# Optimization experiments

Hardware: AMD Instinct MI355X
Metric: run time of the kernel (lower is better)

Reference implementation:

```python
import jax, jax.numpy as jnp
import numpy as np

# --- config mirroring Prediction(__init__) ---
NUM_CLS = 3        # heatmap channels; total C = NUM_CLS + 2 (offset) + 2 (wh)
TOPK = 100         # peaks kept per stack output
SCALE = 4.0        # scale_factor: feature-map stride
CONF_TH = 0.1      # conf_th (also soft-NMS keep thresh, as in forward())
SIGMA = 0.5        # soft-NMS gaussian sigma (default in soft_nms_pytorch)


def setup_inputs() -> dict:
    key = jax.random.key(0)
    # network is identity => x is the raw head output (B, S, C, H, W)
    x = jax.random.normal(key, (32, 2, NUM_CLS + 4, 256, 256), dtype=jnp.float32)
    return {"x": x}


def _decode(hm, off, wh):
    """CenterNet-style hm2box: hm (C,H,W) post-sigmoid, off/wh (2,H,W)."""
    C, H, W = hm.shape
    scores, idx = jax.lax.top_k(hm.reshape(-1), TOPK)      # over C*H*W
    cls = idx // (H * W)
    rem = idx % (H * W)                                    # spatial flat index
    ys = (rem // W).astype(jnp.float32)
    xs = (rem % W).astype(jnp.float32)
    offx = off[0].reshape(-1)[rem]
    offy = off[1].reshape(-1)[rem]
    bw = wh[0].reshape(-1)[rem] * SCALE
    bh = wh[1].reshape(-1)[rem] * SCALE
    cx = (xs + offx) * SCALE
    cy = (ys + offy) * SCALE
    boxes = jnp.stack([cx - bw / 2, cy - bh / 2, cx + bw / 2, cy + bh / 2], axis=-1)
    # conf_th filter: zero-out low scores (fixed shape stand-in for boolean select)
    scores = jnp.where(scores > CONF_TH, scores, 0.0)
    return boxes, cls, scores


def _soft_nms(boxes, scores):
    """Faithful port of soft_nms_pytorch: sequential max-swap + gaussian decay."""
    N = boxes.shape[0]
    pos = jnp.arange(N)

    def step(carry, i):
        bxs, scs, idxs = carry
        # argmax over scores[i:] (includes i; strict '<' in original == first-max here)
        m = jnp.argmax(jnp.where(pos >= i, scs, -jnp.inf))

        def swap(a):
            ai, am = a[i], a[m]
            return a.at[i].set(am).at[m].set(ai)

        bxs, scs, idxs = swap(bxs), swap(scs), swap(idxs)
        bi = bxs[i]
        x1, y1, x2, y2 = bxs[:, 0], bxs[:, 1], bxs[:, 2], bxs[:, 3]
        areas = (x2 - x1 + 1.0) * (y2 - y1 + 1.0)
        area_i = (bi[2] - bi[0] + 1.0) * (bi[3] - bi[1] + 1.0)
        xx1 = jnp.maximum(bi[0], x1)
        yy1 = jnp.maximum(bi[1], y1)
        xx2 = jnp.minimum(bi[2], x2)
        yy2 = jnp.minimum(bi[3], y2)
        inter = jnp.maximum(0.0, xx2 - xx1 + 1.0) * jnp.maximum(0.0, yy2 - yy1 + 1.0)
        iou = inter / (area_i + areas - inter)
        w = jnp.exp(-(iou * iou) / SIGMA)
        scs = jnp.where(pos > i, w * scs, scs)   # decay only positions after i
        return (bxs, scs, idxs), None

    (bxs, scs, idxs), _ = jax.lax.scan(step, (boxes, scores, jnp.arange(N)), jnp.arange(N))
    keep = scs > CONF_TH
    return bxs, scs, idxs, keep


def reference(x):
    b, s, c, H, W = x.shape
    hm = jax.nn.sigmoid(x[:, :, :NUM_CLS])
    off = x[:, :, NUM_CLS:NUM_CLS + 2]
    wh = x[:, :, NUM_CLS + 2:]
    boxes, clss, scores = jax.vmap(jax.vmap(_decode))(hm, off, wh)
    boxes = boxes.reshape(b, s * TOPK, 4)
    clss = clss.reshape(b, s * TOPK)
    scores = scores.reshape(b, s * TOPK)
    nboxes, nscores, idxs, keep = jax.vmap(_soft_nms)(boxes, scores)
    nclss = jnp.take_along_axis(clss, idxs, axis=1)
    # fixed-shape outputs; `keep` marks the boxes the original would return
    return nboxes, nclss, nscores, keep
```

## Files before the change

kernel.cpp:

```cpp
#include <hip/hip_runtime.h>
#include <math.h>

#define TOPK 100
#define HW 65536
#define SLICE_STRIDE (7*HW)
#define NBATCH 32
#define NBOX 200
#define HM (3*HW)
#define CAP 4096
#define NPART 8
#define PPART 64
#define KEYS_BASE 256
#define WS_NEED ((size_t)(2048 + 64 * NPART * PPART * 8))
#define TKEYS 0xC0400000u

__device__ __forceinline__ unsigned fkey(float f) {
    unsigned u = __float_as_uint(f);
    return (u & 0x80000000u) ? ~u : (u | 0x80000000u);
}

__device__ __forceinline__ float sel4(const float a[4], int s) {
    float r = a[0];
    r = (s == 1) ? a[1] : r;
    r = (s == 2) ? a[2] : r;
    r = (s == 3) ? a[3] : r;
    return r;
}

#if defined(__has_builtin) && __has_builtin(__builtin_amdgcn_update_dpp)
#define DPP64_STEP(ctrl)                                                        \
    {                                                                           \
        unsigned lo = (unsigned)x, hi = (unsigned)(x >> 32);                    \
        unsigned olo = (unsigned)__builtin_amdgcn_update_dpp((int)lo, (int)lo,  \
                                                             (ctrl), 0xF, 0xF, false); \
        unsigned ohi = (unsigned)__builtin_amdgcn_update_dpp((int)hi, (int)hi,  \
                                                             (ctrl), 0xF, 0xF, false); \
        unsigned long long o = ((unsigned long long)ohi << 32) | olo;           \
        x = (o > x) ? o : x;                                                    \
    }
__device__ __forceinline__ unsigned long long wave_umax64(unsigned long long x) {
    DPP64_STEP(0x111) DPP64_STEP(0x112) DPP64_STEP(0x114)
    DPP64_STEP(0x118) DPP64_STEP(0x142) DPP64_STEP(0x143)
    unsigned rlo = (unsigned)__builtin_amdgcn_readlane((int)(unsigned)x, 63);
    unsigned rhi = (unsigned)__builtin_amdgcn_readlane((int)(unsigned)(x >> 32), 63);
    return ((unsigned long long)rhi << 32) | rlo;
}
__device__ __forceinline__ float lane_getf(const float a[4], int slot, int lane) {
    return __uint_as_float((unsigned)__builtin_amdgcn_readlane(
        (int)__float_as_uint(sel4(a, slot)), lane));
}
#else
__device__ __forceinline__ unsigned long long wave_umax64(unsigned long long x) {
    #pragma unroll
    for (int off = 32; off > 0; off >>= 1) {
        unsigned long long o = __shfl_xor(x, off);
        if (o > x) x = o;
    }
    return x;
}
__device__ __forceinline__ float lane_getf(const float a[4], int slot, int lane) {
    return __shfl(sel4(a, slot), lane);
}
#endif

typedef __attribute__((ext_vector_type(4))) float f4v;
#if defined(__has_builtin) && __has_builtin(__builtin_nontemporal_load)
#define NT_LOAD(p) __builtin_nontemporal_load(p)
#else
#define NT_LOAD(p) (*(p))
#endif

__global__ __launch_bounds__(1024) void kcollect(const float* __restrict__ x,
                                                 unsigned long long* __restrict__ ws) {
    __shared__ unsigned shCnt;
    const int bid = blockIdx.x;
    const int slice = bid >> 3, part = bid & 7;
    const int t = threadIdx.x;
    const float* xb = x + (size_t)slice * SLICE_STRIDE;
    const f4v* xb4 = (const f4v*)xb;
    unsigned* cnt = (unsigned*)ws;
    unsigned long long* keys = ws + KEYS_BASE;

    if (t == 0) shCnt = 0u;
    __syncthreads();

    const int i0 = part * (HM / 4 / NPART);
    const int i1 = i0 + (HM / 4 / NPART);
    for (int i = i0 + t; i < i1; i += 1024) {
        f4v v = NT_LOAD(&xb4[i]);
        float a[4] = {v.x, v.y, v.z, v.w};
        #pragma unroll
        for (int q = 0; q < 4; ++q) {
            unsigned vk = fkey(a[q]);
            if (vk >= TKEYS) {
                unsigned pos = atomicAdd(&shCnt, 1u);
                if (pos < PPART)
                    keys[(size_t)slice * (NPART * PPART) + part * PPART + pos] =
                        ((unsigned long long)vk << 32) |
                        (unsigned)~(unsigned)(i * 4 + q);
            }
        }
    }
    __syncthreads();
    if (t == 0) cnt[slice * NPART + part] = shCnt;
}

__device__ void fb_select(const float* xb, unsigned long long* fkrow,
                          unsigned* selmask, float* rv, int* ri, int t) {
    for (int i = t; i < HM / 32; i += 1024) selmask[i] = 0u;
    __syncthreads();
    for (int r = 0; r < TOPK; ++r) {
        float bv = -INFINITY; int bi = 0x7FFFFFFF;
        for (int i = t; i < HM; i += 1024) {
            if (!((selmask[i >> 5] >> (i & 31)) & 1u)) {
                float v = xb[i];
                if (v > bv || (v == bv && i < bi)) { bv = v; bi = i; }
            }
        }
        rv[t] = bv; ri[t] = bi;
        __syncthreads();
        for (int off = 512; off > 0; off >>= 1) {
            if (t < off) {
                float ov = rv[t + off]; int oi = ri[t + off];
                if (ov > rv[t] || (ov == rv[t] && oi < ri[t])) { rv[t] = ov; ri[t] = oi; }
            }
            __syncthreads();
        }
        if (t == 0) {
            int w = ri[0];
            selmask[w >> 5] |= (1u << (w & 31));
            fkrow[r] = ((unsigned long long)fkey(rv[0]) << 32) |
                       (unsigned)~(unsigned)w;
        }
        __syncthreads();
    }
}

__global__ __launch_bounds__(1024) void knms6(const float* __restrict__ x,
                                              const unsigned long long* __restrict__ ws,
                                              float* __restrict__ out) {
    __shared__ unsigned long long shpool64[4096];
    __shared__ unsigned long long fk[2][TOPK];
    __shared__ float4 bxs4[NBOX];
    __shared__ float scs[NBOX];
    __shared__ float cl[NBOX];
    __shared__ int badf[2];

    unsigned long long* skey = shpool64;
    unsigned* selmask = (unsigned*)shpool64;
    float* rv = (float*)(selmask + 6144);
    int* ri = (int*)(selmask + 7168);

    const int b = blockIdx.x, t = threadIdx.x;
    const unsigned* cnt = (const unsigned*)ws;
    const unsigned long long* keys = ws + KEYS_BASE;

    if (t < 2) {
        unsigned tot = 0; int bad = 0;
        for (int p8 = 0; p8 < NPART; ++p8) {
            unsigned c = cnt[(2 * b + t) * NPART + p8];
            tot += c;
            if (c > PPART) bad = 1;
        }
        if (tot < TOPK) bad = 1;
        badf[t] = bad;
    }
    __syncthreads();

    if (badf[0]) fb_select(x + (size_t)(2 * b + 0) * SLICE_STRIDE, fk[0],
                           selmask, rv, ri, t);
    if (badf[1]) fb_select(x + (size_t)(2 * b + 1) * SLICE_STRIDE, fk[1],
                           selmask, rv, ri, t);

    const int half = t >> 9, tt = t & 511;
    const int slice = 2 * b + half;
    {
        int part = tt >> 6, off = tt & 63;
        unsigned c = cnt[slice * NPART + part];
        bool valid = (!badf[half]) && ((unsigned)off < c);
        skey[half * 512 + tt] = valid
            ? keys[(size_t)slice * (NPART * PPART) + part * PPART + off] : 0ull;
    }
    __syncthreads();
    for (int k = 2; k <= 512; k <<= 1) {
        for (int j = k >> 1; j > 0; j >>= 1) {
            int i = tt, ixj = i ^ j;
            if (ixj > i) {
                unsigned long long a = skey[half * 512 + i];
                unsigned long long c2 = skey[half * 512 + ixj];
                bool sw = ((i & k) == 0) ? (a < c2) : (a > c2);
                if (sw) { skey[half * 512 + i] = c2; skey[half * 512 + ixj] = a; }
            }
            __syncthreads();
        }
    }

    if (t < NBOX) {
        const int sB = t / TOPK, rank = t - sB * TOPK;
        const int sl2 = 2 * b + sB;
        unsigned long long K = badf[sB] ? fk[sB][rank] : skey[sB * 512 + rank];
        unsigned vk = (unsigned)(K >> 32);
        unsigned idx = ~((unsigned)K);
        unsigned u = (vk & 0x80000000u) ? (vk & 0x7FFFFFFFu) : ~vk;
        float z = __uint_as_float(u);
        int c = (int)(idx >> 16);
        int rem = (int)(idx & 0xFFFFu);
        const float* xb = x + (size_t)sl2 * SLICE_STRIDE;
        float ysf = (float)(rem >> 8);
        float xsf = (float)(rem & 255);
        float offx = xb[3 * HW + rem];
        float offy = xb[4 * HW + rem];
        float bw = xb[5 * HW + rem] * 4.0f;
        float bh = xb[6 * HW + rem] * 4.0f;
        float cx = (xsf + offx) * 4.0f;
        float cy = (ysf + offy) * 4.0f;
        bxs4[t] = make_float4(cx - bw * 0.5f, cy - bh * 0.5f,
                              cx + bw * 0.5f, cy + bh * 0.5f);
        float sg = 1.0f / (1.0f + expf(-z));
        scs[t] = (sg > 0.1f) ? sg : 0.0f;
        cl[t] = (float)c;
    }
    __syncthreads();

    if (t < 64) {
        float X1[4], Y1[4], X2[4], Y2[4], SC[4], CL4[4], AR[4];
        unsigned CP[4];
        #pragma unroll
        for (int sl = 0; sl < 4; ++sl) {
            int p = sl * 64 + t;
            int q = (p < NBOX) ? p : 0;
            float4 bb = bxs4[q];
            X1[sl] = bb.x; Y1[sl] = bb.y; X2[sl] = bb.z; Y2[sl] = bb.w;
            SC[sl] = (p < NBOX) ? scs[q] : 0.0f;
            CL4[sl] = cl[q];
            CP[sl] = (unsigned)p;
            AR[sl] = (X2[sl] - X1[sl] + 1.0f) * (Y2[sl] - Y1[sl] + 1.0f);
        }

        for (int i = 0; i < NBOX; ++i) {
            const unsigned ui = (unsigned)i;
            unsigned long long loc = 0ull;
            #pragma unroll
            for (int sl = 0; sl < 4; ++sl) {
                unsigned cd = ~((CP[sl] << 8) | (unsigned)(sl * 64 + t));
                unsigned long long k =
                    ((unsigned long long)__float_as_uint(SC[sl]) << 32) | cd;
                if (CP[sl] >= ui && k > loc) loc = k;
            }
            unsigned long long kmax = wave_umax64(loc);

            if ((unsigned)(kmax >> 32) == 0u) break;

            unsigned w32 = ~((unsigned)kmax);
            unsigned m = w32 >> 8;
            int worig = (int)(w32 & 0xFFu);
            int lane_m = worig & 63, slot_m = worig >> 6;

            float pvx1 = lane_getf(X1, slot_m, lane_m);
            float pvy1 = lane_getf(Y1, slot_m, lane_m);
            float pvx2 = lane_getf(X2, slot_m, lane_m);
            float pvy2 = lane_getf(Y2, slot_m, lane_m);
            float area_i = lane_getf(AR, slot_m, lane_m);

            #pragma unroll
            for (int sl = 0; sl < 4; ++sl) {
                unsigned cp = CP[sl];
                unsigned ncp = (cp == ui) ? m : cp;
                ncp = (cp == m) ? ui : ncp;
                CP[sl] = ncp;
            }

            float intr[4]; bool anyp = false;
            #pragma unroll
            for (int sl = 0; sl < 4; ++sl) {
                int p = sl * 64 + t;
                bool act = (p < NBOX) && (CP[sl] > ui);
                float xx1 = fmaxf(pvx1, X1[sl]);
                float yy1 = fmaxf(pvy1, Y1[sl]);
                float xx2 = fminf(pvx2, X2[sl]);
                float yy2 = fminf(pvy2, Y2[sl]);
                float inter = fmaxf(0.0f, xx2 - xx1 + 1.0f) *
                              fmaxf(0.0f, yy2 - yy1 + 1.0f);
                intr[sl] = inter;
                anyp |= (act && inter != 0.0f);
            }
            if (__ballot(anyp) != 0ull) {
                #pragma unroll
                for (int sl = 0; sl < 4; ++sl) {
                    int p = sl * 64 + t;
                    if ((p < NBOX) && (CP[sl] > ui)) {
                        float iou = intr[sl] / (area_i + AR[sl] - intr[sl]);
                        float w = expf(-(iou * iou) / 0.5f);
                        SC[sl] = w * SC[sl];
                    }
                }
            }
        }

        float* ob  = out + (size_t)b * NBOX * 4;
        float* oc  = out + (size_t)NBATCH * NBOX * 4 + b * NBOX;
        float* os  = out + (size_t)NBATCH * NBOX * 5 + b * NBOX;
        float* okp = out + (size_t)NBATCH * NBOX * 6 + b * NBOX;
        #pragma unroll
        for (int sl = 0; sl < 4; ++sl) {
            int p = sl * 64 + t;
            if (p < NBOX) {
                unsigned q = CP[sl];
                ob[q * 4 + 0] = X1[sl];
                ob[q * 4 + 1] = Y1[sl];
                ob[q * 4 + 2] = X2[sl];
                ob[q * 4 + 3] = Y2[sl];
                oc[q]  = CL4[sl];
                os[q]  = SC[sl];
                okp[q] = (SC[sl] > 0.1f) ? 1.0f : 0.0f;
            }
        }
    }
}

__global__ __launch_bounds__(1024) void ktopk(const float* __restrict__ x,
                                              float* __restrict__ out) {
    __shared__ unsigned hist[4096];
    __shared__ unsigned long long cand[CAP];
    __shared__ int shB, shB2;
    __shared__ unsigned shAbove, shNcand, shNc;

    const int slice = blockIdx.x;
    const int b = slice >> 1, s = slice & 1;
    const int t = threadIdx.x;
    const float* xb = x + (size_t)slice * SLICE_STRIDE;
    const float4* xb4 = (const float4*)xb;
    const int N4 = HM / 4;

    if (t == 0) { shB = 0; shB2 = 0; shAbove = 0u; shNcand = 0u; shNc = 0u; }
    for (int i = t; i < 4096; i += 1024) hist[i] = 0u;
    __syncthreads();

    for (int i = t; i < N4; i += 1024) {
        float4 v = xb4[i];
        float a[4] = {v.x, v.y, v.z, v.w};
        #pragma unroll
        for (int c_ = 0; c_ < 4; ++c_) {
            unsigned vk = fkey(a[c_]);
            atomicAdd(&hist[vk >> 20], 1u);
        }
    }
    __syncthreads();

    {
        unsigned* tmp = (unsigned*)cand;
        unsigned* src = hist;
        unsigned* dst = tmp;
        for (int d = 1; d < 4096; d <<= 1) {
            for (int i = t; i < 4096; i += 1024) {
                unsigned v = src[i];
                if (i + d < 4096) v += src[i + d];
                dst[i] = v;
            }
            __syncthreads();
            unsigned* sw = src; src = dst; dst = sw;
        }
        for (int i = t; i < 4096; i += 1024) {
            unsigned sb = src[i];
            unsigned sn = (i < 4095) ? src[i + 1] : 0u;
            if (sb >= TOPK && sn < TOPK) { shB = i; shAbove = sn; shNcand = sb; }
        }
        __syncthreads();
    }

    const bool refine = (shNcand > CAP);
    if (refine) {
        for (int i = t; i < 4096; i += 1024) hist[i] = 0u;
        __syncthreads();
        const unsigned Bv = (unsigned)shB;
        for (int i = t; i < N4; i += 1024) {
            float4 v = xb4[i];
            float a[4] = {v.x, v.y, v.z, v.w};
            #pragma unroll
            for (int c_ = 0; c_ < 4; ++c_) {
                unsigned vk = fkey(a[c_]);
                if ((vk >> 20) == Bv) atomicAdd(&hist[(vk >> 8) & 0xFFFu], 1u);
            }
        }
        __syncthreads();
        if (t == 0) {
            unsigned need = TOPK - shAbove, cum = 0u;
            int b2 = 4095;
            for (; b2 >= 0; --b2) { cum += hist[b2]; if (cum >= need) break; }
            shB2 = (b2 < 0) ? 0 : b2;
            shNcand = shAbove + cum;
        }
        __syncthreads();
    }

    {
        const unsigned Bv = (unsigned)shB;
        const unsigned B2v = refine ? (unsigned)shB2 : 0u;
        for (int i = t; i < N4; i += 1024) {
            float4 v = xb4[i];
            float a[4] = {v.x, v.y, v.z, v.w};
            #pragma unroll
            for (int c_ = 0; c_ < 4; ++c_) {
                unsigned vk = fkey(a[c_]);
                unsigned bin = vk >> 20;
                bool q = refine ? (bin > Bv || (bin == Bv && ((vk >> 8) & 0xFFFu) >= B2v))
                                : (bin >= Bv);
                if (q) {
                    unsigned pos = atomicAdd(&shNc, 1u);
                    if (pos < CAP)
                        cand[pos] = ((unsigned long long)vk << 32) |
                                    (unsigned)~(unsigned)(i * 4 + c_);
                }
            }
        }
        __syncthreads();
    }

    unsigned nc = shNc; if (nc > CAP) nc = CAP;
    int P = 128; while (P < (int)nc) P <<= 1;
    for (int i = (int)nc + t; i < P; i += 1024) cand[i] = 0ull;
    __syncthreads();
    for (int k = 2; k <= P; k <<= 1) {
        for (int j = k >> 1; j > 0; j >>= 1) {
            for (int i = t; i < P; i += 1024) {
                int ixj = i ^ j;
                if (ixj > i) {
                    unsigned long long a = cand[i], c2 = cand[ixj];
                    bool sw = ((i & k) == 0) ? (a < c2) : (a > c2);
                    if (sw) { cand[i] = c2; cand[ixj] = a; }
                }
            }
            __syncthreads();
        }
    }

    if (t < TOPK) {
        unsigned long long K = cand[t];
        unsigned vk = (unsigned)(K >> 32);
        unsigned idx = ~((unsigned)K);
        unsigned u = (vk & 0x80000000u) ? (vk & 0x7FFFFFFFu) : ~vk;
        float z = __uint_as_float(u);
        int c = (int)(idx >> 16);
        int rem = (int)(idx & 0xFFFFu);
        float ysf = (float)(rem >> 8);
        float xsf = (float)(rem & 255);
        float offx = xb[3 * HW + rem];
        float offy = xb[4 * HW + rem];
        float bw = xb[5 * HW + rem] * 4.0f;
        float bh = xb[6 * HW + rem] * 4.0f;
        float cx = (xsf + offx) * 4.0f;
        float cy = (ysf + offy) * 4.0f;
        int slot = s * TOPK + t;
        float* ob = out + (size_t)b * NBOX * 4;
        float* oc = out + (size_t)NBATCH * NBOX * 4 + b * NBOX;
        float* os = out + (size_t)NBATCH * NBOX * 5 + b * NBOX;
        ob[slot * 4 + 0] = cx - bw * 0.5f;
        ob[slot * 4 + 1] = cy - bh * 0.5f;
        ob[slot * 4 + 2] = cx + bw * 0.5f;
        ob[slot * 4 + 3] = cy + bh * 0.5f;
        float sg = 1.0f / (1.0f + expf(-z));
        os[slot] = (sg > 0.1f) ? sg : 0.0f;
        oc[slot] = (float)c;
    }
}

__global__ __launch_bounds__(64) void knms(float* __restrict__ out) {
    __shared__ float bxs[NBOX][4];
    __shared__ float scs[NBOX];
    __shared__ float cl[NBOX];

    const int b = blockIdx.x, t = threadIdx.x;
    float* ob  = out + (size_t)b * NBOX * 4;
    float* oc  = out + (size_t)NBATCH * NBOX * 4 + b * NBOX;
    float* os  = out + (size_t)NBATCH * NBOX * 5 + b * NBOX;
    float* okp = out + (size_t)NBATCH * NBOX * 6 + b * NBOX;

    for (int p = t; p < NBOX; p += 64) {
        bxs[p][0] = ob[p * 4 + 0];
        bxs[p][1] = ob[p * 4 + 1];
        bxs[p][2] = ob[p * 4 + 2];
        bxs[p][3] = ob[p * 4 + 3];
        scs[p] = os[p];
        cl[p]  = oc[p];
    }
    __syncthreads();

    unsigned long long local = 0ull;
    for (int p = t; p < NBOX; p += 64) {
        unsigned long long k =
            ((unsigned long long)__float_as_uint(scs[p]) << 32) | (unsigned)~(unsigned)p;
        if (k > local) local = k;
    }
    #pragma unroll
    for (int off = 32; off > 0; off >>= 1) {
        unsigned long long o = __shfl_xor(local, off);
        if (o > local) local = o;
    }
    unsigned long long kmax = local;

    for (int i = 0; i < NBOX; ++i) {
        int m = (int)(~((unsigned)kmax));
        if (t == 0 && m != i) {
            #pragma unroll
            for (int k = 0; k < 4; ++k) {
                float tmp = bxs[i][k]; bxs[i][k] = bxs[m][k]; bxs[m][k] = tmp;
            }
            float ts = scs[i]; scs[i] = scs[m]; scs[m] = ts;
            float tc = cl[i];  cl[i]  = cl[m];  cl[m]  = tc;
        }
        __syncthreads();

        float b0 = bxs[i][0], b1 = bxs[i][1], b2 = bxs[i][2], b3 = bxs[i][3];
        float area_i = (b2 - b0 + 1.0f) * (b3 - b1 + 1.0f);

        local = 0ull;
        for (int p = i + 1 + t; p < NBOX; p += 64) {
            float x1 = bxs[p][0], y1 = bxs[p][1], x2 = bxs[p][2], y2 = bxs[p][3];
            float areas = (x2 - x1 + 1.0f) * (y2 - y1 + 1.0f);
            float xx1 = fmaxf(b0, x1);
            float yy1 = fmaxf(b1, y1);
            float xx2 = fminf(b2, x2);
            float yy2 = fminf(b3, y2);
            float inter = fmaxf(0.0f, xx2 - xx1 + 1.0f) * fmaxf(0.0f, yy2 - yy1 + 1.0f);
            float iou = inter / (area_i + areas - inter);
            float w = expf(-(iou * iou) / 0.5f);
            float ns = w * scs[p];
            scs[p] = ns;
            unsigned long long k =
                ((unsigned long long)__float_as_uint(ns) << 32) | (unsigned)~(unsigned)p;
            if (k > local) local = k;
        }
        __syncthreads();
        #pragma unroll
        for (int off = 32; off > 0; off >>= 1) {
            unsigned long long o = __shfl_xor(local, off);
            if (o > local) local = o;
        }
        kmax = local;
    }
    __syncthreads();

    for (int p = t; p < NBOX; p += 64) {
        ob[p * 4 + 0] = bxs[p][0];
        ob[p * 4 + 1] = bxs[p][1];
        ob[p * 4 + 2] = bxs[p][2];
        ob[p * 4 + 3] = bxs[p][3];
        oc[p]  = cl[p];
        os[p]  = scs[p];
        okp[p] = (scs[p] > 0.1f) ? 1.0f : 0.0f;
    }
}

extern "C" void kernel_launch(void* const* d_in, const int* in_sizes, int n_in,
                              void* d_out, int out_size, void* d_ws, size_t ws_size,
                              hipStream_t stream) {
    const float* x = (const float*)d_in[0];
    float* out = (float*)d_out;
    if (d_ws != nullptr && ws_size >= WS_NEED) {
        kcollect<<<64 * NPART, 1024, 0, stream>>>(x, (unsigned long long*)d_ws);
        knms6<<<NBATCH, 1024, 0, stream>>>(x, (const unsigned long long*)d_ws, out);
    } else {
        ktopk<<<2 * NBATCH, 1024, 0, stream>>>(x, out);
        knms<<<NBATCH, 64, 0, stream>>>(out);
    }
}
```

Baseline: 263.6 us.

## Replace per-step soft-NMS argmax with presorted merge walk plus dirty-set tracking

Precomputes a merged descending order of the two per-stack top-k score lists in shared memory. The soft-NMS loop then walks this order instead of doing a full wave-wide 64-bit max reduction every step. Boxes whose scores were decayed are tracked in dirty bitmasks, and only their maximum is reduced. Ties or zero scores trigger a fallback to the original exact argmax path. This adds bookkeeping (bitmask ballots, readlanes) and branch complexity to the serial 200-step loop.

```diff
diff --git a/kernel.cpp b/kernel.cpp
--- a/kernel.cpp
+++ b/kernel.cpp
@@ -26,6 +26,27 @@
     r = (s == 3) ? a[3] : r;
     return r;
 }
+__device__ __forceinline__ int sel4i(const int a[4], int s) {
+    int r = a[0];
+    r = (s == 1) ? a[1] : r;
+    r = (s == 2) ? a[2] : r;
+    r = (s == 3) ? a[3] : r;
+    return r;
+}
+__device__ __forceinline__ unsigned sel4u(const unsigned a[4], int s) {
+    unsigned r = a[0];
+    r = (s == 1) ? a[1] : r;
+    r = (s == 2) ? a[2] : r;
+    r = (s == 3) ? a[3] : r;
+    return r;
+}
+__device__ __forceinline__ unsigned long long sel4ull(const unsigned long long a[4], int s) {
+    unsigned long long r = a[0];
+    r = (s == 1) ? a[1] : r;
+    r = (s == 2) ? a[2] : r;
+    r = (s == 3) ? a[3] : r;
+    return r;
+}
 
 #if defined(__has_builtin) && __has_builtin(__builtin_amdgcn_update_dpp)
 #define DPP64_STEP(ctrl)                                                        \
@@ -45,6 +66,9 @@
     unsigned rhi = (unsigned)__builtin_amdgcn_readlane((int)(unsigned)(x >> 32), 63);
     return ((unsigned long long)rhi << 32) | rlo;
 }
+__device__ __forceinline__ int lane_geti(int v, int lane) {
+    return __builtin_amdgcn_readlane(v, lane);
+}
 __device__ __forceinline__ float lane_getf(const float a[4], int slot, int lane) {
     return __uint_as_float((unsigned)__builtin_amdgcn_readlane(
         (int)__float_as_uint(sel4(a, slot)), lane));
@@ -58,6 +82,7 @@
     }
     return x;
 }
+__device__ __forceinline__ int lane_geti(int v, int lane) { return __shfl(v, lane); }
 __device__ __forceinline__ float lane_getf(const float a[4], int slot, int lane) {
     return __shfl(sel4(a, slot), lane);
 }
@@ -136,7 +161,7 @@
     }
 }
 
-__global__ __launch_bounds__(1024) void knms6(const float* __restrict__ x,
+__global__ __launch_bounds__(1024) void knms8(const float* __restrict__ x,
                                               const unsigned long long* __restrict__ ws,
                                               float* __restrict__ out) {
     __shared__ unsigned long long shpool64[4096];
@@ -144,7 +169,9 @@
     __shared__ float4 bxs4[NBOX];
     __shared__ float scs[NBOX];
     __shared__ float cl[NBOX];
+    __shared__ int morder[NBOX];
     __shared__ int badf[2];
+    __shared__ int walkBad;
 
     unsigned long long* skey = shpool64;
     unsigned* selmask = (unsigned*)shpool64;
@@ -165,6 +192,7 @@
         if (tot < TOPK) bad = 1;
         badf[t] = bad;
     }
+    if (t == 0) walkBad = 0;
     __syncthreads();
 
     if (badf[0]) fb_select(x + (size_t)(2 * b + 0) * SLICE_STRIDE, fk[0],
@@ -222,9 +250,27 @@
     }
     __syncthreads();
 
+    if (t < NBOX) {
+        const int sB = t / TOPK, rank = t - sB * TOPK;
+        unsigned sb = __float_as_uint(scs[t]);
+        if (sb == 0u) walkBad = 1;
+        if (rank > 0 && __float_as_uint(scs[t - 1]) == sb) walkBad = 1;
+        const int o0 = (1 - sB) * TOPK;
+        int lo = 0, hi = TOPK;
+        while (lo < hi) {
+            int mid = (lo + hi) >> 1;
+            unsigned obt = __float_as_uint(scs[o0 + mid]);
+            if (obt > sb) lo = mid + 1; else hi = mid;
+        }
+        if (lo < TOPK && __float_as_uint(scs[o0 + lo]) == sb) walkBad = 1;
+        morder[rank + lo] = t;
+    }
+    __syncthreads();
+
     if (t < 64) {
         float X1[4], Y1[4], X2[4], Y2[4], SC[4], CL4[4], AR[4];
         unsigned CP[4];
+        int M4[4];
         #pragma unroll
         for (int sl = 0; sl < 4; ++sl) {
             int p = sl * 64 + t;
@@ -235,10 +281,129 @@
             CL4[sl] = cl[q];
             CP[sl] = (unsigned)p;
             AR[sl] = (X2[sl] - X1[sl] + 1.0f) * (Y2[sl] - Y1[sl] + 1.0f);
-        }
+            M4[sl] = (p < NBOX) ? morder[p] : 0;
+        }
+
+        bool useWalk = (walkBad == 0);
+        unsigned long long takenM[4] = {0ull, 0ull, 0ull, 0ull};
+        unsigned long long dirtyM[4] = {0ull, 0ull, 0ull, 0ull};
+        int mi = 0;
+        int Dcnt = 0, Dp = -1;
+        unsigned DmaxSb = 0u;
 
         for (int i = 0; i < NBOX; ++i) {
             const unsigned ui = (unsigned)i;
+
+            if (useWalk) {
+                int fp = -1;
+                while (mi < NBOX) {
+                    int cand2 = lane_geti(sel4i(M4, mi >> 6), mi & 63);
+                    unsigned long long blk =
+                        sel4ull(takenM, cand2 >> 6) | sel4ull(dirtyM, cand2 >> 6);
+                    if ((blk >> (cand2 & 63)) & 1ull) { ++mi; continue; }
+                    fp = cand2; break;
+                }
+                int winner = fp; bool fromD = false;
+                if (Dcnt > 0) {
+                    unsigned fsb = 0u;
+                    if (fp >= 0)
+                        fsb = (unsigned)lane_geti(
+                            (int)__float_as_uint(sel4(SC, fp >> 6)), fp & 63);
+                    if (fp >= 0 && fsb == DmaxSb) {
+                        useWalk = false;
+                    } else if (fp < 0 || DmaxSb > fsb) {
+                        winner = Dp; fromD = true;
+                    }
+                }
+                if (useWalk) {
+                    const int wl = winner & 63, wsl = winner >> 6;
+                    unsigned m = (unsigned)lane_geti((int)sel4u(CP, wsl), wl);
+                    float pvx1 = lane_getf(X1, wsl, wl);
+                    float pvy1 = lane_getf(Y1, wsl, wl);
+                    float pvx2 = lane_getf(X2, wsl, wl);
+                    float pvy2 = lane_getf(Y2, wsl, wl);
+                    float area_i = lane_getf(AR, wsl, wl);
+
+                    #pragma unroll
+                    for (int sl = 0; sl < 4; ++sl) {
+                        unsigned cp = CP[sl];
+                        unsigned ncp = (cp == ui) ? m : cp;
+                        ncp = (cp == m) ? ui : ncp;
+                        CP[sl] = ncp;
+                    }
+                    if (fromD) takenM[wsl] |= (1ull << wl);
+                    else ++mi;
+
+                    float intr[4]; bool act[4]; bool anyp = false;
+                    #pragma unroll
+                    for (int sl = 0; sl < 4; ++sl) {
+                        int p = sl * 64 + t;
+                        act[sl] = (p < NBOX) && (CP[sl] > ui);
+                        float xx1 = fmaxf(pvx1, X1[sl]);
+                        float yy1 = fmaxf(pvy1, Y1[sl]);
+                        float xx2 = fminf(pvx2, X2[sl]);
+                        float yy2 = fminf(pvy2, Y2[sl]);
+                        float inter = fmaxf(0.0f, xx2 - xx1 + 1.0f) *
+                                      fmaxf(0.0f, yy2 - yy1 + 1.0f);
+                        intr[sl] = inter;
+                        anyp |= (act[sl] && inter != 0.0f);
+                    }
+                    bool needD = fromD;
+                    if (__ballot(anyp) != 0ull) {
+                        bool dec[4];
+                        #pragma unroll
+                        for (int sl = 0; sl < 4; ++sl) {
+                            dec[sl] = act[sl] && (intr[sl] != 0.0f);
+                            if (dec[sl]) {
+                                float iou = intr[sl] / (area_i + AR[sl] - intr[sl]);
+                                float w = expf(-(iou * iou) / 0.5f);
+                                SC[sl] = w * SC[sl];
+                            }
+                        }
+                        #pragma unroll
+                        for (int sl = 0; sl < 4; ++sl)
+                            dirtyM[sl] |= __ballot(dec[sl]);
+                        needD = true;
+                    }
+                    if (needD) {
+                        unsigned long long Dm[4];
+                        #pragma unroll
+                        for (int sl = 0; sl < 4; ++sl)
+                            Dm[sl] = dirtyM[sl] & ~takenM[sl];
+                        Dcnt = __popcll(Dm[0]) + __popcll(Dm[1]) +
+                               __popcll(Dm[2]) + __popcll(Dm[3]);
+                        if (Dcnt == 0) { DmaxSb = 0u; Dp = -1; }
+                        else {
+                            unsigned long long loc = 0ull;
+                            bool mem[4];
+                            #pragma unroll
+                            for (int sl = 0; sl < 4; ++sl) {
+                                mem[sl] = (Dm[sl] >> t) & 1ull;
+                                if (mem[sl]) {
+                                    unsigned cd = ~((CP[sl] << 8) |
+                                                    (unsigned)(sl * 64 + t));
+                                    unsigned long long kk =
+                                        ((unsigned long long)
+                                         __float_as_uint(SC[sl]) << 32) | cd;
+                                    if (kk > loc) loc = kk;
+                                }
+                            }
+                            unsigned long long kd = wave_umax64(loc);
+                            DmaxSb = (unsigned)(kd >> 32);
+                            Dp = (int)((~((unsigned)kd)) & 0xFFu);
+                            int lt = 0;
+                            #pragma unroll
+                            for (int sl = 0; sl < 4; ++sl)
+                                if (mem[sl] && __float_as_uint(SC[sl]) == DmaxSb) ++lt;
+                            unsigned long long b1 = __ballot(lt >= 1);
+                            unsigned long long b2 = __ballot(lt >= 2);
+                            if (b2 != 0ull || __popcll(b1) > 1) useWalk = false;
+                        }
+                    }
+                    continue;
+                }
+            }
+
             unsigned long long loc = 0ull;
             #pragma unroll
             for (int sl = 0; sl < 4; ++sl) {
@@ -248,7 +413,6 @@
                 if (CP[sl] >= ui && k > loc) loc = k;
             }
             unsigned long long kmax = wave_umax64(loc);
-
             if ((unsigned)(kmax >> 32) == 0u) break;
 
             unsigned w32 = ~((unsigned)kmax);
@@ -274,7 +438,7 @@
             #pragma unroll
             for (int sl = 0; sl < 4; ++sl) {
                 int p = sl * 64 + t;
-                bool act = (p < NBOX) && (CP[sl] > ui);
+                bool act2 = (p < NBOX) && (CP[sl] > ui);
                 float xx1 = fmaxf(pvx1, X1[sl]);
                 float yy1 = fmaxf(pvy1, Y1[sl]);
                 float xx2 = fminf(pvx2, X2[sl]);
@@ -282,7 +446,7 @@
                 float inter = fmaxf(0.0f, xx2 - xx1 + 1.0f) *
                               fmaxf(0.0f, yy2 - yy1 + 1.0f);
                 intr[sl] = inter;
-                anyp |= (act && inter != 0.0f);
+                anyp |= (act2 && inter != 0.0f);
             }
             if (__ballot(anyp) != 0ull) {
                 #pragma unroll
@@ -558,7 +722,7 @@
     float* out = (float*)d_out;
     if (d_ws != nullptr && ws_size >= WS_NEED) {
         kcollect<<<64 * NPART, 1024, 0, stream>>>(x, (unsigned long long*)d_ws);
-        knms6<<<NBATCH, 1024, 0, stream>>>(x, (const unsigned long long*)d_ws, out);
+        knms8<<<NBATCH, 1024, 0, stream>>>(x, (const unsigned long long*)d_ws, out);
     } else {
         ktopk<<<2 * NBATCH, 1024, 0, stream>>>(x, out);
         knms<<<NBATCH, 64, 0, stream>>>(out);
```

Measured after the change: 280.8 us. +6.5%, slower.
